# Optimization experiments

Measured on AMD Instinct MI355X. Metric: run time of the kernel, lower is better.

Reference implementation:

```python
import jax, jax.numpy as jnp
import numpy as np

FUZZY_FACTOR = 2
REG_WT = 0.0008


def setup_inputs() -> dict:
    key = jax.random.key(0)
    k1, k2 = jax.random.split(key)
    logits = jax.random.normal(k1, (2, 4, 128, 128, 128), dtype=jnp.float32)
    y_pred = jax.nn.softmax(logits, axis=1)  # module assumes softmax already applied
    image = jax.random.normal(k2, (2, 1, 128, 128, 128), dtype=jnp.float32)
    return {"y_pred": y_pred, "image": image}


def _neighbor_sum(x):
    # x: [B, K, D, H, W]; 3x3x3 ones kernel with zero center, SAME padding,
    # applied independently per (batch, cluster) channel.
    B, K, D, H, W = x.shape
    kernel = jnp.ones((1, 1, 3, 3, 3), x.dtype).at[0, 0, 1, 1, 1].set(0.0)
    y = jax.lax.conv_general_dilated(
        x.reshape(B * K, 1, D, H, W), kernel,
        window_strides=(1, 1, 1), padding="SAME",
        dimension_numbers=("NCDHW", "OIDHW", "NCDHW"))
    return y.reshape(B, K, D, H, W)


def reference(y_pred, image):
    B, K = y_pred.shape[0], y_pred.shape[1]
    N = int(np.prod(y_pred.shape[2:]))
    pred = y_pred.reshape(B, K, N)          # [B, K, N]
    img = image.reshape(B, N)               # [B, N]

    mem = pred ** FUZZY_FACTOR              # fuzzy memberships [B, K, N]

    # cluster centroids v_k = sum(img*mem)/sum(mem)  -> [B, K]
    v = jnp.sum(img[:, None, :] * mem, axis=2) / jnp.sum(mem, axis=2)

    # J_1 = sum_i mem_i * (img - v_i)^2   -> [B, N]
    J1 = jnp.sum(mem * (img[:, None, :] - v[:, :, None]) ** 2, axis=1)

    # neighbor sum of each cluster's membership map (box filter minus center)
    nb = _neighbor_sum(mem.reshape(y_pred.shape)).reshape(B, K, N)
    # sum over j != i, computed once as total - self (identical algebra)
    J_in = jnp.sum(nb, axis=1, keepdims=True) - nb  # [B, K, N]
    J2 = jnp.sum(mem * J_in, axis=1)                # [B, N]

    return jnp.mean(J1) + REG_WT * jnp.mean(J2)
```

## Files before the change

### kernel.cpp

```cpp
#include <hip/hip_runtime.h>


#define BB 2
#define KK 4
#define DD 128
#define HH 128
#define WW 128
#define PLANE (HH * WW)
#define SD 8
#define NBD (DD / SD)
#define HR 8
#define NBH (HH / HR)
#define NT 256
#define LROW 128
#define LPL (10 * LROW)
#define LBUF (KK * LPL)

typedef const void __attribute__((address_space(1))) gvoid_t;
typedef void __attribute__((address_space(3))) svoid_t;
#define GLD(gp, lp) __builtin_amdgcn_global_load_lds((gvoid_t*)(gp), (svoid_t*)(lp), 16, 0, 0)

#define PIPE_BARRIER() asm volatile("s_waitcnt vmcnt(5) lgkmcnt(0)\n\ts_barrier" ::: "memory")
#define ISSUE_FENCE()  asm volatile("" ::: "memory")

__global__ __launch_bounds__(NT) void rfcm_main(
    const float* __restrict__ yp, const float* __restrict__ img,
    double* __restrict__ ws)
{
    __shared__ __align__(16) float sbuf[4 * LBUF];

    const int tid = threadIdx.x;
    const int wl  = tid & 31;
    const int hr  = tid >> 5;
    const int c0  = wl << 2;

    const int bid  = blockIdx.x;
    const int xcd  = bid & 7;
    const int idx  = bid >> 3;
    const int sl   = idx >> 4;
    const int ht   = idx & 15;
    const int slab = sl * 8 + xcd;
    const int b    = slab >> 4;
    const int dsb  = slab & 15;

    const int h0 = ht * HR;
    const int d0 = dsb * SD;
    const int h  = h0 + hr;

    const int wv = tid >> 6;
    const int L  = tid & 63;
    const int rr = L >> 5;
    const int cl = (L & 31) << 2;

    auto dma_plane = [&](int t, int slot) {
        if ((unsigned)t >= (unsigned)DD) return;
        const float* pb = yp + (size_t)((b * KK + wv) * DD + t) * PLANE;
        #pragma unroll
        for (int c = 0; c < 5; c++) {
            const int r = (c << 1) + rr;
            int g = h0 - 1 + r;
            g = g < 0 ? 0 : (g > HH - 1 ? HH - 1 : g);
            const float* gp = pb + g * WW + cl;
            float* lp = &sbuf[slot * LBUF + wv * LPL + (c << 1) * LROW];
            GLD(gp, lp);
        }
    };

    const bool okL = (wl > 0), okR = (wl < 31);
    const float msc = (h > 0)      ? 1.f : 0.f;
    const float psc = (h < HH - 1) ? 1.f : 0.f;

    auto extract = [&](int slot, int k, float4& s9, float4& mm) {
        const float* p3 = &sbuf[slot * LBUF + k * LPL + hr * LROW + c0];
        const float4 a4 = *(const float4*)(p3);
        const float4 b4 = *(const float4*)(p3 + LROW);
        const float4 c4 = *(const float4*)(p3 + 2 * LROW);
        const float4 sb = make_float4(b4.x*b4.x, b4.y*b4.y, b4.z*b4.z, b4.w*b4.w);
        mm = sb;
        float4 v;
        v.x = fmaf(a4.x*a4.x, msc, fmaf(c4.x*c4.x, psc, sb.x));
        v.y = fmaf(a4.y*a4.y, msc, fmaf(c4.y*c4.y, psc, sb.y));
        v.z = fmaf(a4.z*a4.z, msc, fmaf(c4.z*c4.z, psc, sb.z));
        v.w = fmaf(a4.w*a4.w, msc, fmaf(c4.w*c4.w, psc, sb.w));
        const float vL = okL ? __shfl_up(v.w, 1)   : 0.f;
        const float vR = okR ? __shfl_down(v.x, 1) : 0.f;
        s9.x = vL  + v.x + v.y;
        s9.y = v.x + v.y + v.z;
        s9.z = v.y + v.z + v.w;
        s9.w = v.z + v.w + vR;
    };

    const float* imgb = img + (size_t)b * DD * PLANE + h * WW + c0;

    dma_plane(d0 - 1, 0);
    dma_plane(d0,     1);
    float4 iv = *(const float4*)(imgb + (size_t)d0 * PLANE);
    ISSUE_FENCE();
    dma_plane(d0 + 1, 2);
    dma_plane(d0 + 2, 3);
    asm volatile("s_waitcnt vmcnt(10) lgkmcnt(0)\n\ts_barrier" ::: "memory");

    float4 s9p[KK], s9c[KK], mc[KK], dum;
    const bool vprev = (d0 > 0);
    #pragma unroll
    for (int k = 0; k < KK; k++) {
        if (vprev) extract(0, k, s9p[k], dum);
        else       s9p[k] = make_float4(0.f, 0.f, 0.f, 0.f);
        extract(1, k, s9c[k], mc[k]);
    }

    float smf[KK] = {0,0,0,0}, sif[KK] = {0,0,0,0}, saf[KK] = {0,0,0,0};
    float j2f = 0.f;

    #pragma unroll
    for (int i = 0; i < SD; i++) {
        const int d = d0 + i;
        PIPE_BARRIER();

        float4 ivn = iv;
        if (i < SD - 1) ivn = *(const float4*)(imgb + (size_t)(d + 1) * PLANE);
        ISSUE_FENCE();
        if (i < SD - 2) dma_plane(d + 3, i & 3);

        const bool vn = (d + 1 < DD);
        const float4 iv2 = make_float4(iv.x*iv.x, iv.y*iv.y, iv.z*iv.z, iv.w*iv.w);

        float4 summ  = make_float4(0.f, 0.f, 0.f, 0.f);
        float4 sumbk = make_float4(0.f, 0.f, 0.f, 0.f);
        float4 cross = make_float4(0.f, 0.f, 0.f, 0.f);

        #pragma unroll
        for (int k = 0; k < KK; k++) {
            float4 s9n, mn;
            if (vn) extract((i + 2) & 3, k, s9n, mn);
            else { s9n = make_float4(0.f,0.f,0.f,0.f); mn = s9n; }

            const float4 m = mc[k];
            float4 bk;
            bk.x = s9p[k].x + s9c[k].x + s9n.x;
            bk.y = s9p[k].y + s9c[k].y + s9n.y;
            bk.z = s9p[k].z + s9c[k].z + s9n.z;
            bk.w = s9p[k].w + s9c[k].w + s9n.w;

            summ.x += m.x; summ.y += m.y; summ.z += m.z; summ.w += m.w;
            sumbk.x += bk.x; sumbk.y += bk.y; sumbk.z += bk.z; sumbk.w += bk.w;
            cross.x = fmaf(m.x, bk.x - m.x, cross.x);
            cross.y = fmaf(m.y, bk.y - m.y, cross.y);
            cross.z = fmaf(m.z, bk.z - m.z, cross.z);
            cross.w = fmaf(m.w, bk.w - m.w, cross.w);

            smf[k] += (m.x + m.y) + (m.z + m.w);
            sif[k] = fmaf(m.x, iv.x,  fmaf(m.y, iv.y,  fmaf(m.z, iv.z,  fmaf(m.w, iv.w,  sif[k]))));
            saf[k] = fmaf(m.x, iv2.x, fmaf(m.y, iv2.y, fmaf(m.z, iv2.z, fmaf(m.w, iv2.w, saf[k]))));

            s9p[k] = s9c[k]; s9c[k] = s9n; mc[k] = mn;
        }

        j2f += (summ.x * (sumbk.x - summ.x) - cross.x)
             + (summ.y * (sumbk.y - summ.y) - cross.y)
             + (summ.z * (sumbk.z - summ.z) - cross.z)
             + (summ.w * (sumbk.w - summ.w) - cross.w);

        iv = ivn;
    }

    double q[13];
    #pragma unroll
    for (int k = 0; k < KK; k++) {
        q[k] = (double)smf[k]; q[4 + k] = (double)sif[k]; q[8 + k] = (double)saf[k];
    }
    q[12] = (double)j2f;

    #pragma unroll
    for (int qq = 0; qq < 13; qq++) {
        double v = q[qq];
        #pragma unroll
        for (int off = 32; off > 0; off >>= 1) v += __shfl_down(v, off, 64);
        q[qq] = v;
    }

    __syncthreads();
    double* red = (double*)sbuf;
    const int lane = tid & 63, wid = tid >> 6;
    if (lane == 0) {
        #pragma unroll
        for (int qq = 0; qq < 13; qq++) red[wid * 13 + qq] = q[qq];
    }
    __syncthreads();
    if (tid < 13) {
        const double sfin = red[tid] + red[13 + tid] + red[26 + tid] + red[39 + tid];
        int idxo;
        if      (tid < 4)  idxo = b * KK + tid;
        else if (tid < 8)  idxo = 8  + b * KK + (tid - 4);
        else if (tid < 12) idxo = 16 + b * KK + (tid - 8);
        else               idxo = 24;
        unsafeAtomicAdd(&ws[idxo], sfin);
    }
}

__global__ void rfcm_fin(const double* __restrict__ ws, float* __restrict__ out)
{
    if (threadIdx.x == 0 && blockIdx.x == 0) {
        double j1 = 0;
        #pragma unroll
        for (int i = 0; i < BB * KK; i++)
            j1 += ws[16 + i] - ws[8 + i] * ws[8 + i] / ws[i];
        const double invBN = 1.0 / ((double)BB * (double)DD * (double)HH * (double)WW);
        out[0] = (float)(j1 * invBN + 0.0008 * ws[24] * invBN);
    }
}

extern "C" void kernel_launch(void* const* d_in, const int* in_sizes, int n_in,
                              void* d_out, int out_size, void* d_ws, size_t ws_size,
                              hipStream_t stream) {
    const float* yp  = (const float*)d_in[0];
    const float* img = (const float*)d_in[1];
    float* out = (float*)d_out;
    double* ws = (double*)d_ws;

    hipMemsetAsync(d_ws, 0, 25 * sizeof(double), stream);

    dim3 grid(BB * NBD * NBH);
    rfcm_main<<<grid, NT, 0, stream>>>(yp, img, ws);
    rfcm_fin<<<1, 64, 0, stream>>>(ws, out);
}
```

Baseline: 139.9 us.

## Give each wave private double-buffered LDS slices and drop block-wide barriers

Each wave now DMAs only its own two output rows plus halo for all four clusters into a private two-slot LDS buffer. Per-iteration synchronisation becomes a per-wave vmcnt(0) wait instead of a block-wide s_barrier. This removes cross-wave barrier stalls and shrinks the LDS footprint, which may allow more resident blocks. In exchange, the prefetch depth drops from two planes ahead to one, the wait also blocks on the image load, and the outer loop is only partially unrolled.

```diff
diff --git a/kernel.cpp b/kernel.cpp
--- a/kernel.cpp
+++ b/kernel.cpp
@@ -12,26 +12,25 @@
 #define HR 8
 #define NBH (HH / HR)
 #define NT 256
-#define LROW 128
-#define LPL (10 * LROW)
-#define LBUF (KK * LPL)
+#define SLROW 128
+#define SLICE (KK * 4 * SLROW)
 
 typedef const void __attribute__((address_space(1))) gvoid_t;
 typedef void __attribute__((address_space(3))) svoid_t;
 #define GLD(gp, lp) __builtin_amdgcn_global_load_lds((gvoid_t*)(gp), (svoid_t*)(lp), 16, 0, 0)
-
-#define PIPE_BARRIER() asm volatile("s_waitcnt vmcnt(5) lgkmcnt(0)\n\ts_barrier" ::: "memory")
-#define ISSUE_FENCE()  asm volatile("" ::: "memory")
+#define WAIT_VM0() __builtin_amdgcn_s_waitcnt(0x0F70)
 
 __global__ __launch_bounds__(NT) void rfcm_main(
     const float* __restrict__ yp, const float* __restrict__ img,
     double* __restrict__ ws)
 {
-    __shared__ __align__(16) float sbuf[4 * LBUF];
+    __shared__ __align__(16) float sbuf[4 * 2 * SLICE];
 
     const int tid = threadIdx.x;
-    const int wl  = tid & 31;
-    const int hr  = tid >> 5;
+    const int wv  = tid >> 6;
+    const int L   = tid & 63;
+    const int wl  = L & 31;
+    const int hy  = L >> 5;
     const int c0  = wl << 2;
 
     const int bid  = blockIdx.x;
@@ -43,26 +42,30 @@
     const int b    = slab >> 4;
     const int dsb  = slab & 15;
 
-    const int h0 = ht * HR;
-    const int d0 = dsb * SD;
-    const int h  = h0 + hr;
-
-    const int wv = tid >> 6;
-    const int L  = tid & 63;
+    const int h0  = ht * HR;
+    const int hp0 = h0 + (wv << 1);
+    const int h   = hp0 + hy;
+    const int d0  = dsb * SD;
+
+    float* const mybuf = &sbuf[wv * 2 * SLICE];
+
     const int rr = L >> 5;
     const int cl = (L & 31) << 2;
 
-    auto dma_plane = [&](int t, int slot) {
+    auto dma_batch = [&](int t) {
         if ((unsigned)t >= (unsigned)DD) return;
-        const float* pb = yp + (size_t)((b * KK + wv) * DD + t) * PLANE;
-        #pragma unroll
-        for (int c = 0; c < 5; c++) {
-            const int r = (c << 1) + rr;
-            int g = h0 - 1 + r;
-            g = g < 0 ? 0 : (g > HH - 1 ? HH - 1 : g);
-            const float* gp = pb + g * WW + cl;
-            float* lp = &sbuf[slot * LBUF + wv * LPL + (c << 1) * LROW];
-            GLD(gp, lp);
+        float* const bb = mybuf + (t & 1) * SLICE;
+        #pragma unroll
+        for (int k = 0; k < KK; k++) {
+            const float* pb = yp + (size_t)((b * KK + k) * DD + t) * PLANE;
+            #pragma unroll
+            for (int rp = 0; rp < 2; rp++) {
+                int g = hp0 - 1 + (rp << 1) + rr;
+                g = g < 0 ? 0 : (g > HH - 1 ? HH - 1 : g);
+                const float* gp = pb + g * WW + cl;
+                float* lp = bb + (k * 4 + (rp << 1)) * SLROW;
+                GLD(gp, lp);
+            }
         }
     };
 
@@ -70,11 +73,11 @@
     const float msc = (h > 0)      ? 1.f : 0.f;
     const float psc = (h < HH - 1) ? 1.f : 0.f;
 
-    auto extract = [&](int slot, int k, float4& s9, float4& mm) {
-        const float* p3 = &sbuf[slot * LBUF + k * LPL + hr * LROW + c0];
+    auto extract = [&](int t, int k, float4& s9, float4& mm) {
+        const float* p3 = mybuf + (t & 1) * SLICE + (k * 4 + hy) * SLROW + c0;
         const float4 a4 = *(const float4*)(p3);
-        const float4 b4 = *(const float4*)(p3 + LROW);
-        const float4 c4 = *(const float4*)(p3 + 2 * LROW);
+        const float4 b4 = *(const float4*)(p3 + SLROW);
+        const float4 c4 = *(const float4*)(p3 + 2 * SLROW);
         const float4 sb = make_float4(b4.x*b4.x, b4.y*b4.y, b4.z*b4.z, b4.w*b4.w);
         mm = sb;
         float4 v;
@@ -92,36 +95,32 @@
 
     const float* imgb = img + (size_t)b * DD * PLANE + h * WW + c0;
 
-    dma_plane(d0 - 1, 0);
-    dma_plane(d0,     1);
+    dma_batch(d0 - 1);
+    dma_batch(d0);
     float4 iv = *(const float4*)(imgb + (size_t)d0 * PLANE);
-    ISSUE_FENCE();
-    dma_plane(d0 + 1, 2);
-    dma_plane(d0 + 2, 3);
-    asm volatile("s_waitcnt vmcnt(10) lgkmcnt(0)\n\ts_barrier" ::: "memory");
+    WAIT_VM0();
 
     float4 s9p[KK], s9c[KK], mc[KK], dum;
     const bool vprev = (d0 > 0);
     #pragma unroll
     for (int k = 0; k < KK; k++) {
-        if (vprev) extract(0, k, s9p[k], dum);
+        if (vprev) extract(d0 - 1, k, s9p[k], dum);
         else       s9p[k] = make_float4(0.f, 0.f, 0.f, 0.f);
-        extract(1, k, s9c[k], mc[k]);
-    }
+        extract(d0, k, s9c[k], mc[k]);
+    }
+    dma_batch(d0 + 1);
 
     float smf[KK] = {0,0,0,0}, sif[KK] = {0,0,0,0}, saf[KK] = {0,0,0,0};
     float j2f = 0.f;
 
-    #pragma unroll
+    #pragma unroll 2
     for (int i = 0; i < SD; i++) {
         const int d = d0 + i;
-        PIPE_BARRIER();
+        WAIT_VM0();
 
         float4 ivn = iv;
         if (i < SD - 1) ivn = *(const float4*)(imgb + (size_t)(d + 1) * PLANE);
-        ISSUE_FENCE();
-        if (i < SD - 2) dma_plane(d + 3, i & 3);
-
+        if (i <= SD - 2) dma_batch(d + 2);
         const bool vn = (d + 1 < DD);
         const float4 iv2 = make_float4(iv.x*iv.x, iv.y*iv.y, iv.z*iv.z, iv.w*iv.w);
 
@@ -132,7 +131,7 @@
         #pragma unroll
         for (int k = 0; k < KK; k++) {
             float4 s9n, mn;
-            if (vn) extract((i + 2) & 3, k, s9n, mn);
+            if (vn) extract(d + 1, k, s9n, mn);
             else { s9n = make_float4(0.f,0.f,0.f,0.f); mn = s9n; }
 
             const float4 m = mc[k];
```

Result: faster. 122.4 us (-12.6%).
